# Performance work log

Hardware: AMD Instinct MI355X
Metric: run time of the kernel (lower is better)

## Reference

```python
import jax, jax.numpy as jnp
import numpy as np

N = 50000
E = 800000
F_IN = 128
HID = 16
HEADS = 8
C = 16
NEG_SLOPE = 0.2


def setup_inputs() -> dict:
    key = jax.random.key(0)
    ks = jax.random.split(key, 12)
    glorot = lambda k, shape: jax.random.normal(k, shape, jnp.float32) * jnp.sqrt(2.0 / (shape[0] + shape[-1]))
    return {
        "x": jax.random.normal(ks[0], (N, F_IN), jnp.float32),
        "edge_index": jax.random.randint(ks[1], (2, E), 0, N, jnp.int32),
        "x2": jax.random.normal(ks[2], (N, F_IN), jnp.float32),
        "edge_index2": jax.random.randint(ks[3], (2, E), 0, N, jnp.int32),
        # conv1: GATConv(F_IN -> HID, heads=HEADS, concat=True)
        "W1": glorot(ks[4], (F_IN, HEADS * HID)),
        "a1_src": glorot(ks[5], (HEADS, HID)),
        "a1_dst": glorot(ks[6], (HEADS, HID)),
        "b1": jnp.zeros((HEADS * HID,), jnp.float32),
        # conv2: GATConv(HEADS*HID -> C, heads=1, concat=False)
        "W2": glorot(ks[7], (HEADS * HID, 1 * C)),
        "a2_src": glorot(ks[8], (1, C)),
        "a2_dst": glorot(ks[9], (1, C)),
        "b2": jnp.zeros((C,), jnp.float32),
    }


def gat_conv(x, edge_index, W, a_src, a_dst, bias, concat):
    """PyG-style GATConv with self-loops, segment softmax over destinations."""
    n = x.shape[0]
    heads, out = a_src.shape
    h = (x @ W).reshape(n, heads, out)               # [N, H, O]
    loops = jnp.arange(n, dtype=edge_index.dtype)
    src = jnp.concatenate([edge_index[0], loops])     # messages flow src -> dst
    dst = jnp.concatenate([edge_index[1], loops])
    alpha_s = jnp.einsum('nho,ho->nh', h, a_src)
    alpha_d = jnp.einsum('nho,ho->nh', h, a_dst)
    e = jax.nn.leaky_relu(alpha_s[src] + alpha_d[dst], NEG_SLOPE)  # [E+N, H]
    m = jax.lax.stop_gradient(jax.ops.segment_max(e, dst, num_segments=n))
    w = jnp.exp(e - m[dst])
    denom = jax.ops.segment_sum(w, dst, num_segments=n)
    alpha = w / (denom[dst] + 1e-16)                  # segment softmax
    msg = h[src] * alpha[:, :, None]                  # [E+N, H, O]
    agg = jax.ops.segment_sum(msg, dst, num_segments=n)
    agg = agg.reshape(n, heads * out) if concat else agg.mean(axis=1)
    return agg + bias


def forward_once(x, edge_index, W1, a1_src, a1_dst, b1, W2, a2_src, a2_dst, b2):
    # dropout(p=0.6) is identity in eval mode
    h = jax.nn.elu(gat_conv(x, edge_index, W1, a1_src, a1_dst, b1, concat=True))
    return gat_conv(h, edge_index, W2, a2_src, a2_dst, b2, concat=False)


def reference(x, edge_index, x2, edge_index2, W1, a1_src, a1_dst, b1, W2, a2_src, a2_dst, b2):
    y = forward_once(x, edge_index, W1, a1_src, a1_dst, b1, W2, a2_src, a2_dst, b2)
    z = forward_once(x2, edge_index2, W1, a1_src, a1_dst, b1, W2, a2_src, a2_dst, b2)
    eps = 1e-8
    ny = jnp.maximum(jnp.linalg.norm(y, axis=1), eps)
    nz = jnp.maximum(jnp.linalg.norm(z, axis=1), eps)
    cos = jnp.sum(y * z, axis=1) / (ny * nz)
    ls_y = jax.nn.log_softmax(y, axis=1)
    ls_z = jax.nn.log_softmax(z, axis=1)
    return (ls_y, 1.0 - cos, ls_z, ls_y, ls_y)
```

## Files before the change

### kernel.cpp

```cpp
#include <hip/hip_runtime.h>
#include <hip/hip_bf16.h>

#define N_NODES 50000
#define N_EDGES 800000
#define F_INS   128
#define HIDDEN  16
#define HEADS   8
#define HO      128
#define C_OUT   16
#define NEG_SLOPE 0.2f
#define SLOT    64
#define NB_G1X  ((N_NODES + 31) / 32)
#define XSTR    132

#define NCLS     128
#define CLS_MUL  1342u
#define CLS_SH   19
#define CAP      8192
#define CHUNK    2048
#define NB_BKT   ((N_EDGES + CHUNK - 1) / CHUNK)

typedef unsigned short u16;
typedef unsigned int   u32;
typedef int v4i __attribute__((ext_vector_type(4)));

__device__ __forceinline__ float bf2f(u16 u) {
    union { u32 i; float f; } t; t.i = ((u32)u) << 16; return t.f;
}
__device__ __forceinline__ float bflo(u32 q) {
    union { u32 i; float f; } t; t.i = q << 16; return t.f;
}
__device__ __forceinline__ float bfhi(u32 q) {
    union { u32 i; float f; } t; t.i = q & 0xFFFF0000u; return t.f;
}
__device__ __forceinline__ u16 f2bf(float f) {
    union { float f; u32 i; } t; t.f = f;
    u32 x = t.i;
    u32 lsb = (x >> 16) & 1u;
    x += 0x7FFFu + lsb;
    return (u16)(x >> 16);
}
__device__ __forceinline__ int cls_of(int d) { return (int)(((u32)d * CLS_MUL) >> CLS_SH); }
__host__ __device__ __forceinline__ int cls_base(int c) { return (int)(((u32)c * 524288u + (CLS_MUL - 1)) / CLS_MUL); }

__launch_bounds__(256)
__global__ void k_bucket(const int* __restrict__ ei0, const int* __restrict__ ei1,
                         int* __restrict__ gcur, u32* __restrict__ bucket) {
    __shared__ int cnt[NCLS];
    __shared__ int base[NCLS];
    int t = threadIdx.x;
    int g = blockIdx.x & 1;
    int chunk = blockIdx.x >> 1;
    int e0 = chunk * CHUNK + t * 8;
    bool act = e0 < N_EDGES;

    if (t < NCLS) cnt[t] = 0;
    __syncthreads();

    const int* src = g ? ei1 : ei0;
    const int* dst = src + N_EDGES;
    int d8[8], s8[8], c8[8];
    if (act) {
        v4i da = *(const v4i*)(dst + e0), db = *(const v4i*)(dst + e0 + 4);
        v4i sa = *(const v4i*)(src + e0), sb = *(const v4i*)(src + e0 + 4);
        d8[0]=da[0]; d8[1]=da[1]; d8[2]=da[2]; d8[3]=da[3];
        d8[4]=db[0]; d8[5]=db[1]; d8[6]=db[2]; d8[7]=db[3];
        s8[0]=sa[0]; s8[1]=sa[1]; s8[2]=sa[2]; s8[3]=sa[3];
        s8[4]=sb[0]; s8[5]=sb[1]; s8[6]=sb[2]; s8[7]=sb[3];
        #pragma unroll
        for (int j = 0; j < 8; ++j) {
            c8[j] = cls_of(d8[j]);
            atomicAdd(&cnt[c8[j]], 1);
        }
    }
    __syncthreads();
    if (t < NCLS) {
        int n = cnt[t];
        base[t] = n ? atomicAdd(&gcur[g * NCLS + t], n) : 0;
        cnt[t] = 0;
    }
    __syncthreads();
    if (act) {
        #pragma unroll
        for (int j = 0; j < 8; ++j) {
            int c = c8[j];
            int p = atomicAdd(&cnt[c], 1);
            bucket[(size_t)(g * NCLS + c) * CAP + base[c] + p] =
                ((u32)d8[j] << 16) | (u32)s8[j];
        }
    }
}

__launch_bounds__(256)
__global__ void k_build(const int* __restrict__ gcur, const u32* __restrict__ bucket,
                        int* __restrict__ cursor, u16* __restrict__ col) {
    __shared__ int cnt[391];
    int t = threadIdx.x;
    int c = blockIdx.x & (NCLS - 1);
    int g = blockIdx.x >> 7;
    int d0 = cls_base(c);
    int d1 = (c == NCLS - 1) ? N_NODES : cls_base(c + 1);
    int nn = d1 - d0;
    for (int j = t; j < nn; j += 256) cnt[j] = 0;
    __syncthreads();

    int size = gcur[g * NCLS + c];
    const u32* bp = bucket + (size_t)(g * NCLS + c) * CAP;
    u16* cl = col + (size_t)g * N_NODES * SLOT;
    for (int i = t; i < size; i += 256) {
        u32 e = bp[i];
        int d = (int)(e >> 16);
        int s = (int)(e & 0xFFFFu);
        int p = atomicAdd(&cnt[d - d0], 1);
        if (p < SLOT) cl[(size_t)d * SLOT + p] = (u16)s;
    }
    __syncthreads();
    int* cur = cursor + g * N_NODES;
    for (int j = t; j < nn; j += 256) cur[d0 + j] = cnt[j];
}

__launch_bounds__(256)
__global__ void k_gemm1(const float* __restrict__ x, const float* __restrict__ W1,
                        const float* __restrict__ a1s, const float* __restrict__ a1d,
                        u32* __restrict__ h1b, float* __restrict__ as_,
                        float* __restrict__ ad_) {
    __shared__ float ws_[F_INS * 64];
    __shared__ float xs[32 * XSTR];
    int t = threadIdx.x;
    int half = blockIdx.y;

    const float4* w4 = (const float4*)W1;
    float4*       wl = (float4*)ws_;
    #pragma unroll
    for (int i = 0; i < 8; ++i) {
        int id2 = t + i * 256;
        int k = id2 >> 4;
        int c = id2 & 15;
        wl[id2] = w4[k * 32 + half * 16 + c];
    }

    int r0 = blockIdx.x * 32;
    const float4* x4 = (const float4*)x;
    #pragma unroll
    for (int i = 0; i < 4; ++i) {
        int id2 = t + i * 256;
        int r  = id2 >> 5;
        int c4 = id2 & 31;
        float4 q = make_float4(0.f, 0.f, 0.f, 0.f);
        if (r0 + r < N_NODES) q = x4[(size_t)(r0 + r) * 32 + c4];
        *(float4*)(xs + r * XSTR + c4 * 4) = q;
    }
    __syncthreads();

    int cg = t & 15;
    int rs = t >> 4;
    float acc[2][4];
    #pragma unroll
    for (int i = 0; i < 2; ++i)
        #pragma unroll
        for (int j = 0; j < 4; ++j) acc[i][j] = 0.f;

    #pragma unroll 8
    for (int k = 0; k < F_INS; ++k) {
        float4 wv = wl[k * 16 + cg];
        float xv0 = xs[rs * XSTR + k];
        float xv1 = xs[(rs + 16) * XSTR + k];
        acc[0][0] += xv0 * wv.x; acc[0][1] += xv0 * wv.y;
        acc[0][2] += xv0 * wv.z; acc[0][3] += xv0 * wv.w;
        acc[1][0] += xv1 * wv.x; acc[1][1] += xv1 * wv.y;
        acc[1][2] += xv1 * wv.z; acc[1][3] += xv1 * wv.w;
    }

    int gc = half * 64 + 4 * cg;
    int hglob = gc >> 4;
    float4 va = *(const float4*)(a1s + gc);
    float4 vd = *(const float4*)(a1d + gc);

    #pragma unroll
    for (int i = 0; i < 2; ++i) {
        int r = r0 + rs + 16 * i;
        float sa = acc[i][0]*va.x + acc[i][1]*va.y + acc[i][2]*va.z + acc[i][3]*va.w;
        float sd = acc[i][0]*vd.x + acc[i][1]*vd.y + acc[i][2]*vd.z + acc[i][3]*vd.w;
        sa += __shfl_xor(sa, 1); sa += __shfl_xor(sa, 2);
        sd += __shfl_xor(sd, 1); sd += __shfl_xor(sd, 2);
        if (r < N_NODES) {
            u32 p0 = ((u32)f2bf(acc[i][1]) << 16) | (u32)f2bf(acc[i][0]);
            u32 p1 = ((u32)f2bf(acc[i][3]) << 16) | (u32)f2bf(acc[i][2]);
            ((uint2*)h1b)[(size_t)r * 32 + half * 16 + cg] = make_uint2(p0, p1);
            if ((cg & 3) == 0) {
                as_[r * 8 + hglob] = sa;
                ad_[r * 8 + hglob] = sd;
            }
        }
    }
}

__launch_bounds__(256)
__global__ void k_gat1(const u32* __restrict__ h1b, const float* __restrict__ as_,
                       const float* __restrict__ ad_, const int* __restrict__ cursor,
                       const u16* __restrict__ col, const float* __restrict__ b1,
                       u32* __restrict__ hL1) {
    int lane = threadIdx.x & 63;
    int node = blockIdx.x * 4 + (threadIdx.x >> 6);
    if (node >= N_NODES) return;
    int h = lane >> 3;
    float ad = ad_[node * 8 + h];

    float as0 = as_[node * 8 + h];
    float tt = as0 + ad;
    tt = (tt > 0.f) ? tt : NEG_SLOPE * tt;
    float w = __expf(tt);
    float denom = w;
    u32 q = h1b[(size_t)node * 64 + lane];
    float ax = w * bflo(q), ay = w * bfhi(q);

    int deg = min(cursor[node], SLOT);
    const u16* cp = col + (size_t)node * SLOT;
    int e = 0;
    for (; e + 7 < deg; e += 8) {
        ushort4 sa4 = *(const ushort4*)(cp + e);
        ushort4 sb4 = *(const ushort4*)(cp + e + 4);
        int s0 = sa4.x, s1 = sa4.y, s2 = sa4.z, s3 = sa4.w;
        int s4 = sb4.x, s5 = sb4.y, s6 = sb4.z, s7 = sb4.w;
        float A0 = as_[s0 * 8 + h], A1 = as_[s1 * 8 + h];
        float A2 = as_[s2 * 8 + h], A3 = as_[s3 * 8 + h];
        float A4 = as_[s4 * 8 + h], A5 = as_[s5 * 8 + h];
        float A6 = as_[s6 * 8 + h], A7 = as_[s7 * 8 + h];
        u32 q0 = h1b[(size_t)s0 * 64 + lane], q1 = h1b[(size_t)s1 * 64 + lane];
        u32 q2 = h1b[(size_t)s2 * 64 + lane], q3 = h1b[(size_t)s3 * 64 + lane];
        u32 q4 = h1b[(size_t)s4 * 64 + lane], q5 = h1b[(size_t)s5 * 64 + lane];
        u32 q6 = h1b[(size_t)s6 * 64 + lane], q7 = h1b[(size_t)s7 * 64 + lane];
        float t0 = A0 + ad; t0 = (t0 > 0.f) ? t0 : NEG_SLOPE * t0;
        float t1 = A1 + ad; t1 = (t1 > 0.f) ? t1 : NEG_SLOPE * t1;
        float t2 = A2 + ad; t2 = (t2 > 0.f) ? t2 : NEG_SLOPE * t2;
        float t3 = A3 + ad; t3 = (t3 > 0.f) ? t3 : NEG_SLOPE * t3;
        float t4 = A4 + ad; t4 = (t4 > 0.f) ? t4 : NEG_SLOPE * t4;
        float t5 = A5 + ad; t5 = (t5 > 0.f) ? t5 : NEG_SLOPE * t5;
        float t6 = A6 + ad; t6 = (t6 > 0.f) ? t6 : NEG_SLOPE * t6;
        float t7 = A7 + ad; t7 = (t7 > 0.f) ? t7 : NEG_SLOPE * t7;
        float w0 = __expf(t0), w1 = __expf(t1), w2 = __expf(t2), w3 = __expf(t3);
        float w4 = __expf(t4), w5 = __expf(t5), w6 = __expf(t6), w7 = __expf(t7);
        denom += ((w0 + w1) + (w2 + w3)) + ((w4 + w5) + (w6 + w7));
        ax += w0 * bflo(q0) + w1 * bflo(q1) + w2 * bflo(q2) + w3 * bflo(q3)
            + w4 * bflo(q4) + w5 * bflo(q5) + w6 * bflo(q6) + w7 * bflo(q7);
        ay += w0 * bfhi(q0) + w1 * bfhi(q1) + w2 * bfhi(q2) + w3 * bfhi(q3)
            + w4 * bfhi(q4) + w5 * bfhi(q5) + w6 * bfhi(q6) + w7 * bfhi(q7);
    }
    for (; e + 3 < deg; e += 4) {
        ushort4 s4v = *(const ushort4*)(cp + e);
        int s0 = s4v.x, s1 = s4v.y, s2 = s4v.z, s3 = s4v.w;
        float A0 = as_[s0 * 8 + h], A1 = as_[s1 * 8 + h];
        float A2 = as_[s2 * 8 + h], A3 = as_[s3 * 8 + h];
        u32 q0 = h1b[(size_t)s0 * 64 + lane], q1 = h1b[(size_t)s1 * 64 + lane];
        u32 q2 = h1b[(size_t)s2 * 64 + lane], q3 = h1b[(size_t)s3 * 64 + lane];
        float t0 = A0 + ad; t0 = (t0 > 0.f) ? t0 : NEG_SLOPE * t0;
        float t1 = A1 + ad; t1 = (t1 > 0.f) ? t1 : NEG_SLOPE * t1;
        float t2 = A2 + ad; t2 = (t2 > 0.f) ? t2 : NEG_SLOPE * t2;
        float t3 = A3 + ad; t3 = (t3 > 0.f) ? t3 : NEG_SLOPE * t3;
        float w0 = __expf(t0), w1 = __expf(t1), w2 = __expf(t2), w3 = __expf(t3);
        denom += (w0 + w1) + (w2 + w3);
        ax += w0 * bflo(q0) + w1 * bflo(q1) + w2 * bflo(q2) + w3 * bflo(q3);
        ay += w0 * bfhi(q0) + w1 * bfhi(q1) + w2 * bfhi(q2) + w3 * bfhi(q3);
    }
    for (; e < deg; ++e) {
        int s = cp[e];
        float A = as_[s * 8 + h];
        u32 qq = h1b[(size_t)s * 64 + lane];
        float t0 = A + ad; t0 = (t0 > 0.f) ? t0 : NEG_SLOPE * t0;
        float w0 = __expf(t0);
        denom += w0;
        ax += w0 * bflo(qq);
        ay += w0 * bfhi(qq);
    }
    float inv = 1.f / (denom + 1e-16f);
    int c = lane * 2;
    float o0 = ax * inv + b1[c];
    float o1 = ay * inv + b1[c + 1];
    o0 = (o0 > 0.f) ? o0 : (__expf(o0) - 1.f);
    o1 = (o1 > 0.f) ? o1 : (__expf(o1) - 1.f);
    hL1[(size_t)node * 64 + lane] = ((u32)f2bf(o1) << 16) | (u32)f2bf(o0);
}

__launch_bounds__(256)
__global__ void k_gemm2(const u16* __restrict__ hL1, const float* __restrict__ W2,
                        const float* __restrict__ a2s, const float* __restrict__ a2d,
                        float* __restrict__ h2, float* __restrict__ as2,
                        float* __restrict__ ad2) {
    __shared__ float w2s[F_INS * C_OUT];
    __shared__ float hs[16 * 136];
    int t = threadIdx.x;

    const float4* w4 = (const float4*)W2;
    #pragma unroll
    for (int i = 0; i < 2; ++i) {
        int idx = t + i * 256;
        ((float4*)w2s)[idx] = w4[idx];
    }
    int r0 = blockIdx.x * 16;
    const ushort4* hg = (const ushort4*)hL1;
    #pragma unroll
    for (int i = 0; i < 2; ++i) {
        int idx = t + i * 256;
        int r  = idx >> 5;
        int c4 = idx & 31;
        ushort4 q = make_ushort4(0, 0, 0, 0);
        if (r0 + r < N_NODES) q = hg[(size_t)(r0 + r) * 32 + c4];
        float4 v; v.x = bf2f(q.x); v.y = bf2f(q.y); v.z = bf2f(q.z); v.w = bf2f(q.w);
        *(float4*)(hs + r * 136 + c4 * 4) = v;
    }
    __syncthreads();

    int c = t & 15, r = t >> 4;
    float acc = 0.f;
    #pragma unroll 8
    for (int k = 0; k < F_INS; ++k) acc += hs[r * 136 + k] * w2s[k * C_OUT + c];
    int n = r0 + r;
    if (n < N_NODES) h2[(size_t)n * C_OUT + c] = acc;

    float sa = acc * a2s[c];
    float sd = acc * a2d[c];
    #pragma unroll
    for (int m = 1; m < 16; m <<= 1) {
        sa += __shfl_xor(sa, m);
        sd += __shfl_xor(sd, m);
    }
    if (c == 0 && n < N_NODES) { as2[n] = sa; ad2[n] = sd; }
}

__device__ __forceinline__ void gat2_accum(const float* __restrict__ h2,
                                           const float* __restrict__ as2, float ad,
                                           const u16* __restrict__ cp, int deg, int c,
                                           float& denom, float& acc) {
    int e = 0;
    for (; e + 7 < deg; e += 8) {
        ushort4 sa4 = *(const ushort4*)(cp + e);
        ushort4 sb4 = *(const ushort4*)(cp + e + 4);
        int s0 = sa4.x, s1 = sa4.y, s2 = sa4.z, s3 = sa4.w;
        int s4 = sb4.x, s5 = sb4.y, s6 = sb4.z, s7 = sb4.w;
        float A0 = as2[s0], A1 = as2[s1], A2 = as2[s2], A3 = as2[s3];
        float A4 = as2[s4], A5 = as2[s5], A6 = as2[s6], A7 = as2[s7];
        float v0 = h2[(size_t)s0 * C_OUT + c], v1 = h2[(size_t)s1 * C_OUT + c];
        float v2 = h2[(size_t)s2 * C_OUT + c], v3 = h2[(size_t)s3 * C_OUT + c];
        float v4 = h2[(size_t)s4 * C_OUT + c], v5 = h2[(size_t)s5 * C_OUT + c];
        float v6 = h2[(size_t)s6 * C_OUT + c], v7 = h2[(size_t)s7 * C_OUT + c];
        float t0 = A0 + ad; t0 = (t0 > 0.f) ? t0 : NEG_SLOPE * t0;
        float t1 = A1 + ad; t1 = (t1 > 0.f) ? t1 : NEG_SLOPE * t1;
        float t2 = A2 + ad; t2 = (t2 > 0.f) ? t2 : NEG_SLOPE * t2;
        float t3 = A3 + ad; t3 = (t3 > 0.f) ? t3 : NEG_SLOPE * t3;
        float t4 = A4 + ad; t4 = (t4 > 0.f) ? t4 : NEG_SLOPE * t4;
        float t5 = A5 + ad; t5 = (t5 > 0.f) ? t5 : NEG_SLOPE * t5;
        float t6 = A6 + ad; t6 = (t6 > 0.f) ? t6 : NEG_SLOPE * t6;
        float t7 = A7 + ad; t7 = (t7 > 0.f) ? t7 : NEG_SLOPE * t7;
        float w0 = __expf(t0), w1 = __expf(t1), w2 = __expf(t2), w3 = __expf(t3);
        float w4 = __expf(t4), w5 = __expf(t5), w6 = __expf(t6), w7 = __expf(t7);
        denom += ((w0 + w1) + (w2 + w3)) + ((w4 + w5) + (w6 + w7));
        acc += (w0 * v0 + w1 * v1 + w2 * v2 + w3 * v3)
             + (w4 * v4 + w5 * v5 + w6 * v6 + w7 * v7);
    }
    for (; e + 3 < deg; e += 4) {
        ushort4 s4v = *(const ushort4*)(cp + e);
        int s0 = s4v.x, s1 = s4v.y, s2 = s4v.z, s3 = s4v.w;
        float A0 = as2[s0], A1 = as2[s1], A2 = as2[s2], A3 = as2[s3];
        float v0 = h2[(size_t)s0 * C_OUT + c], v1 = h2[(size_t)s1 * C_OUT + c];
        float v2 = h2[(size_t)s2 * C_OUT + c], v3 = h2[(size_t)s3 * C_OUT + c];
        float t0 = A0 + ad; t0 = (t0 > 0.f) ? t0 : NEG_SLOPE * t0;
        float t1 = A1 + ad; t1 = (t1 > 0.f) ? t1 : NEG_SLOPE * t1;
        float t2 = A2 + ad; t2 = (t2 > 0.f) ? t2 : NEG_SLOPE * t2;
        float t3 = A3 + ad; t3 = (t3 > 0.f) ? t3 : NEG_SLOPE * t3;
        float w0 = __expf(t0), w1 = __expf(t1), w2 = __expf(t2), w3 = __expf(t3);
        denom += (w0 + w1) + (w2 + w3);
        acc += w0 * v0 + w1 * v1 + w2 * v2 + w3 * v3;
    }
    for (; e < deg; ++e) {
        int s = cp[e];
        float t0 = as2[s] + ad; t0 = (t0 > 0.f) ? t0 : NEG_SLOPE * t0;
        float w0 = __expf(t0);
        denom += w0;
        acc += w0 * h2[(size_t)s * C_OUT + c];
    }
}

__launch_bounds__(256)
__global__ void k_gat2(const float* __restrict__ h2, const float* __restrict__ as2,
                       const float* __restrict__ ad2, const int* __restrict__ cursor,
                       const u16* __restrict__ col, const float* __restrict__ b2,
                       float* __restrict__ yout) {
    int t = threadIdx.x;
    int node = blockIdx.x * 16 + (t >> 4);
    int c = t & 15;
    if (node >= N_NODES) return;
    float ad = ad2[node];

    float tt = as2[node] + ad;
    tt = (tt > 0.f) ? tt : NEG_SLOPE * tt;
    float w = __expf(tt);
    float denom = w;
    float acc = w * h2[(size_t)node * C_OUT + c];

    int deg = min(cursor[node], SLOT);
    gat2_accum(h2, as2, ad, col + (size_t)node * SLOT, deg, c, denom, acc);
    yout[(size_t)node * C_OUT + c] = acc / (denom + 1e-16f) + b2[c];
}

__launch_bounds__(256)
__global__ void k_gat2f(const float* __restrict__ h2, const float* __restrict__ as2,
                        const float* __restrict__ ad2, const int* __restrict__ cursor,
                        const u16* __restrict__ col, const float* __restrict__ b2,
                        const float* __restrict__ yb, float* __restrict__ out) {
    int t = threadIdx.x;
    int node = blockIdx.x * 16 + (t >> 4);
    int c = t & 15;
    if (node >= N_NODES) return;
    float ad = ad2[node];

    float tt = as2[node] + ad;
    tt = (tt > 0.f) ? tt : NEG_SLOPE * tt;
    float w = __expf(tt);
    float denom = w;
    float acc = w * h2[(size_t)node * C_OUT + c];

    int deg = min(cursor[node], SLOT);
    gat2_accum(h2, as2, ad, col + (size_t)node * SLOT, deg, c, denom, acc);
    float zv = acc / (denom + 1e-16f) + b2[c];
    float yv = yb[(size_t)node * C_OUT + c];

    float my = yv, mz = zv;
    #pragma unroll
    for (int m = 1; m < 16; m <<= 1) {
        my = fmaxf(my, __shfl_xor(my, m));
        mz = fmaxf(mz, __shfl_xor(mz, m));
    }
    float sy = __expf(yv - my), sz = __expf(zv - mz);
    float dot = yv * zv, ny = yv * yv, nz = zv * zv;
    #pragma unroll
    for (int m = 1; m < 16; m <<= 1) {
        sy  += __shfl_xor(sy, m);
        sz  += __shfl_xor(sz, m);
        dot += __shfl_xor(dot, m);
        ny  += __shfl_xor(ny, m);
        nz  += __shfl_xor(nz, m);
    }
    float lsey = my + __logf(sy);
    float lsez = mz + __logf(sz);
    float omc = 1.f - dot / (fmaxf(sqrtf(ny), 1e-8f) * fmaxf(sqrtf(nz), 1e-8f));

    const int O1 = N_NODES * C_OUT;
    const int O2 = O1 + N_NODES;
    const int O3 = O2 + N_NODES * C_OUT;
    const int O4 = O3 + N_NODES * C_OUT;
    float ly = yv - lsey;
    float lz = zv - lsez;
    int base = node * 16 + c;
    out[base]      = ly;
    out[O2 + base] = lz;
    out[O3 + base] = ly;
    out[O4 + base] = ly;
    if (c == 0) out[O1 + node] = omc;
}

extern "C" void kernel_launch(void* const* d_in, const int* in_sizes, int n_in,
                              void* d_out, int out_size, void* d_ws, size_t ws_size,
                              hipStream_t stream) {
    (void)in_sizes; (void)n_in; (void)out_size; (void)ws_size;
    const float* x1  = (const float*)d_in[0];
    const int*   ei1 = (const int*)d_in[1];
    const float* x2  = (const float*)d_in[2];
    const int*   ei2 = (const int*)d_in[3];
    const float* W1  = (const float*)d_in[4];
    const float* a1s = (const float*)d_in[5];
    const float* a1d = (const float*)d_in[6];
    const float* b1  = (const float*)d_in[7];
    const float* W2  = (const float*)d_in[8];
    const float* a2s = (const float*)d_in[9];
    const float* a2d = (const float*)d_in[10];
    const float* b2  = (const float*)d_in[11];
    float* out = (float*)d_out;

    char* p = (char*)d_ws;
    int* gcur      = (int*)p; p += (size_t)2 * NCLS * 4;
    int* cursor    = (int*)p; p += (size_t)2 * N_NODES * 4;
    u16* col       = (u16*)p; p += (size_t)2 * N_NODES * SLOT * 2;
    float* as1  = (float*)p; p += (size_t)N_NODES * HEADS * 4;
    float* ad1  = (float*)p; p += (size_t)N_NODES * HEADS * 4;
    float* h2   = (float*)p; p += (size_t)N_NODES * C_OUT * 4;
    float* as2  = (float*)p; p += (size_t)N_NODES * 4;
    float* ad2  = (float*)p; p += (size_t)N_NODES * 4;
    float* yb   = (float*)p; p += (size_t)N_NODES * C_OUT * 4;
    u32* hL1    = (u32*)p;   p += (size_t)N_NODES * HO * 2;
    u32* h1b    = (u32*)p;   p += (size_t)N_NODES * HO * 2;
    u32* bucket = h1b;

    hipMemsetAsync(gcur, 0, (size_t)2 * NCLS * 4, stream);
    k_bucket<<<2 * NB_BKT, 256, 0, stream>>>(ei1, ei2, gcur, bucket);
    k_build <<<2 * NCLS, 256, 0, stream>>>(gcur, bucket, cursor, col);

    for (int g = 0; g < 2; ++g) {
        const float* x = g ? x2 : x1;
        int* cur_g = cursor + g * N_NODES;
        u16* col_g = col + (size_t)g * N_NODES * SLOT;
        dim3 g1(NB_G1X, 2);
        k_gemm1<<<g1, 256, 0, stream>>>(x, W1, a1s, a1d, h1b, as1, ad1);
        k_gat1 <<<(N_NODES + 3) / 4, 256, 0, stream>>>(h1b, as1, ad1, cur_g, col_g, b1, hL1);
        k_gemm2<<<(N_NODES + 15) / 16, 256, 0, stream>>>((const u16*)hL1, W2, a2s, a2d, h2, as2, ad2);
        if (g == 0) {
            k_gat2 <<<(N_NODES + 15) / 16, 256, 0, stream>>>(h2, as2, ad2, cur_g, col_g, b2, yb);
        } else {
            k_gat2f<<<(N_NODES + 15) / 16, 256, 0, stream>>>(h2, as2, ad2, cur_g, col_g, b2, yb, out);
        }
    }
}
```

Baseline: 342.9 us.

## Compute first-layer GEMM with bf16 MFMA and fold attention vectors into weights

Replaces the fp32 SIMT GEMM for layer 1 with a bf16 MFMA 16x16x32 kernel. A small prep kernel transposes and packs W1 to bf16 and precomputes W1·a_src and W1·a_dst as an extra 16-column tile, so the attention logits come straight out of the same MFMA pass. Each block now handles 64 rows across all 128 columns, so x is read once instead of twice. In exchange, x and the attention projections are rounded to bf16, which lowers accuracy of the attention scores.

```diff
diff --git a/kernel.cpp b/kernel.cpp
--- a/kernel.cpp
+++ b/kernel.cpp
@@ -10,8 +10,7 @@
 #define C_OUT   16
 #define NEG_SLOPE 0.2f
 #define SLOT    64
-#define NB_G1X  ((N_NODES + 31) / 32)
-#define XSTR    132
+#define NB_G1   ((N_NODES + 63) / 64)
 
 #define NCLS     128
 #define CLS_MUL  1342u
@@ -23,6 +22,8 @@
 typedef unsigned short u16;
 typedef unsigned int   u32;
 typedef int v4i __attribute__((ext_vector_type(4)));
+typedef short bf16x8 __attribute__((ext_vector_type(8)));
+typedef float f32x4 __attribute__((ext_vector_type(4)));
 
 __device__ __forceinline__ float bf2f(u16 u) {
     union { u32 i; float f; } t; t.i = ((u32)u) << 16; return t.f;
@@ -33,15 +34,43 @@
 __device__ __forceinline__ float bfhi(u32 q) {
     union { u32 i; float f; } t; t.i = q & 0xFFFF0000u; return t.f;
 }
-__device__ __forceinline__ u16 f2bf(float f) {
+__device__ __forceinline__ u32 f2bf(float f) {
     union { float f; u32 i; } t; t.f = f;
     u32 x = t.i;
     u32 lsb = (x >> 16) & 1u;
     x += 0x7FFFu + lsb;
-    return (u16)(x >> 16);
+    return x >> 16;
 }
 __device__ __forceinline__ int cls_of(int d) { return (int)(((u32)d * CLS_MUL) >> CLS_SH); }
 __host__ __device__ __forceinline__ int cls_base(int c) { return (int)(((u32)c * 524288u + (CLS_MUL - 1)) / CLS_MUL); }
+
+__global__ void k_wt(const float* __restrict__ W1, const float* __restrict__ a1s,
+                     const float* __restrict__ a1d, u32* __restrict__ w1t,
+                     u32* __restrict__ a1t) {
+    int t = threadIdx.x;
+    if (blockIdx.x < 32) {
+        int e = blockIdx.x * 256 + t;
+        int c = e >> 6, kp = e & 63;
+        float lo = W1[(2 * kp) * 128 + c];
+        float hi = W1[(2 * kp + 1) * 128 + c];
+        w1t[e] = (f2bf(hi) << 16) | f2bf(lo);
+    } else {
+        #pragma unroll
+        for (int i = 0; i < 4; ++i) {
+            int wi = t + i * 256;
+            int n = wi >> 6, kp = wi & 63;
+            int h = n >> 1;
+            const float* av = ((n & 1) ? a1d : a1s) + h * 16;
+            float s0 = 0.f, s1 = 0.f;
+            #pragma unroll
+            for (int c = 0; c < 16; ++c) {
+                s0 += W1[(2 * kp) * 128 + h * 16 + c] * av[c];
+                s1 += W1[(2 * kp + 1) * 128 + h * 16 + c] * av[c];
+            }
+            a1t[wi] = (f2bf(s1) << 16) | f2bf(s0);
+        }
+    }
+}
 
 __launch_bounds__(256)
 __global__ void k_bucket(const int* __restrict__ ei0, const int* __restrict__ ei1,
@@ -120,77 +149,67 @@
 }
 
 __launch_bounds__(256)
-__global__ void k_gemm1(const float* __restrict__ x, const float* __restrict__ W1,
-                        const float* __restrict__ a1s, const float* __restrict__ a1d,
-                        u32* __restrict__ h1b, float* __restrict__ as_,
-                        float* __restrict__ ad_) {
-    __shared__ float ws_[F_INS * 64];
-    __shared__ float xs[32 * XSTR];
-    int t = threadIdx.x;
-    int half = blockIdx.y;
-
-    const float4* w4 = (const float4*)W1;
-    float4*       wl = (float4*)ws_;
-    #pragma unroll
-    for (int i = 0; i < 8; ++i) {
-        int id2 = t + i * 256;
-        int k = id2 >> 4;
-        int c = id2 & 15;
-        wl[id2] = w4[k * 32 + half * 16 + c];
-    }
-
-    int r0 = blockIdx.x * 32;
-    const float4* x4 = (const float4*)x;
-    #pragma unroll
-    for (int i = 0; i < 4; ++i) {
-        int id2 = t + i * 256;
-        int r  = id2 >> 5;
-        int c4 = id2 & 31;
-        float4 q = make_float4(0.f, 0.f, 0.f, 0.f);
-        if (r0 + r < N_NODES) q = x4[(size_t)(r0 + r) * 32 + c4];
-        *(float4*)(xs + r * XSTR + c4 * 4) = q;
-    }
-    __syncthreads();
-
-    int cg = t & 15;
-    int rs = t >> 4;
-    float acc[2][4];
-    #pragma unroll
-    for (int i = 0; i < 2; ++i)
+__global__ void k_gemm1(const float* __restrict__ x, const u32* __restrict__ w1t,
+                        const u32* __restrict__ a1t, u32* __restrict__ h1b,
+                        float* __restrict__ as_, float* __restrict__ ad_) {
+    __shared__ u32 xls[4096];
+    int t = threadIdx.x;
+    int r0 = blockIdx.x * 64;
+
+    const float2* x2p = (const float2*)x;
+    #pragma unroll
+    for (int i = 0; i < 16; ++i) {
+        int A = t + i * 256;
+        int wi = A >> 10, kt = (A >> 8) & 3, L = (A >> 2) & 63, jj = A & 3;
+        int m = L & 15, qd = L >> 4;
+        int r = r0 + wi * 16 + m;
+        int pp = kt * 16 + qd * 4 + jj;
+        float2 v = make_float2(0.f, 0.f);
+        if (r < N_NODES) v = x2p[(size_t)r * 64 + pp];
+        xls[A] = (f2bf(v.y) << 16) | f2bf(v.x);
+    }
+    __syncthreads();
+
+    int lane = t & 63;
+    int wid = t >> 6;
+    int n = lane & 15, quad = lane >> 4;
+
+    f32x4 acc[8], acca;
+    #pragma unroll
+    for (int ct = 0; ct < 8; ++ct) acc[ct] = (f32x4){0.f, 0.f, 0.f, 0.f};
+    acca = (f32x4){0.f, 0.f, 0.f, 0.f};
+
+    #pragma unroll
+    for (int kt = 0; kt < 4; ++kt) {
+        union { uint4 u; bf16x8 v; } af;
+        af.u = *(const uint4*)(xls + wid * 1024 + kt * 256 + lane * 4);
         #pragma unroll
-        for (int j = 0; j < 4; ++j) acc[i][j] = 0.f;
-
-    #pragma unroll 8
-    for (int k = 0; k < F_INS; ++k) {
-        float4 wv = wl[k * 16 + cg];
-        float xv0 = xs[rs * XSTR + k];
-        float xv1 = xs[(rs + 16) * XSTR + k];
-        acc[0][0] += xv0 * wv.x; acc[0][1] += xv0 * wv.y;
-        acc[0][2] += xv0 * wv.z; acc[0][3] += xv0 * wv.w;
-        acc[1][0] += xv1 * wv.x; acc[1][1] += xv1 * wv.y;
-        acc[1][2] += xv1 * wv.z; acc[1][3] += xv1 * wv.w;
-    }
-
-    int gc = half * 64 + 4 * cg;
-    int hglob = gc >> 4;
-    float4 va = *(const float4*)(a1s + gc);
-    float4 vd = *(const float4*)(a1d + gc);
-
-    #pragma unroll
-    for (int i = 0; i < 2; ++i) {
-        int r = r0 + rs + 16 * i;
-        float sa = acc[i][0]*va.x + acc[i][1]*va.y + acc[i][2]*va.z + acc[i][3]*va.w;
-        float sd = acc[i][0]*vd.x + acc[i][1]*vd.y + acc[i][2]*vd.z + acc[i][3]*vd.w;
-        sa += __shfl_xor(sa, 1); sa += __shfl_xor(sa, 2);
-        sd += __shfl_xor(sd, 1); sd += __shfl_xor(sd, 2);
-        if (r < N_NODES) {
-            u32 p0 = ((u32)f2bf(acc[i][1]) << 16) | (u32)f2bf(acc[i][0]);
-            u32 p1 = ((u32)f2bf(acc[i][3]) << 16) | (u32)f2bf(acc[i][2]);
-            ((uint2*)h1b)[(size_t)r * 32 + half * 16 + cg] = make_uint2(p0, p1);
-            if ((cg & 3) == 0) {
-                as_[r * 8 + hglob] = sa;
-                ad_[r * 8 + hglob] = sd;
-            }
+        for (int ct = 0; ct < 8; ++ct) {
+            union { uint4 u; bf16x8 v; } bf_;
+            bf_.u = *(const uint4*)(w1t + (ct * 16 + n) * 64 + kt * 16 + quad * 4);
+            acc[ct] = __builtin_amdgcn_mfma_f32_16x16x32_bf16(af.v, bf_.v, acc[ct], 0, 0, 0);
+        }
+        union { uint4 u; bf16x8 v; } ba;
+        ba.u = *(const uint4*)(a1t + n * 64 + kt * 16 + quad * 4);
+        acca = __builtin_amdgcn_mfma_f32_16x16x32_bf16(af.v, ba.v, acca, 0, 0, 0);
+    }
+
+    int h = n >> 1;
+    #pragma unroll
+    for (int reg = 0; reg < 4; ++reg) {
+        int gr = r0 + wid * 16 + quad * 4 + reg;
+        bool ok = gr < N_NODES;
+        float av = acca[reg];
+        if (ok) {
+            if (n & 1) ad_[gr * 8 + h] = av;
+            else       as_[gr * 8 + h] = av;
+        }
+        #pragma unroll
+        for (int ct = 0; ct < 8; ++ct) {
+            u32 my = f2bf(acc[ct][reg]);
+            u32 ot = (u32)__shfl_xor((int)my, 1);
+            if (!(n & 1) && ok)
+                h1b[(size_t)gr * 64 + ct * 8 + (n >> 1)] = (ot << 16) | my;
         }
     }
 }
@@ -278,7 +297,7 @@
     float o1 = ay * inv + b1[c + 1];
     o0 = (o0 > 0.f) ? o0 : (__expf(o0) - 1.f);
     o1 = (o1 > 0.f) ? o1 : (__expf(o1) - 1.f);
-    hL1[(size_t)node * 64 + lane] = ((u32)f2bf(o1) << 16) | (u32)f2bf(o0);
+    hL1[(size_t)node * 64 + lane] = (f2bf(o1) << 16) | f2bf(o0);
 }
 
 __launch_bounds__(256)
@@ -478,6 +497,8 @@
 
     char* p = (char*)d_ws;
     int* gcur      = (int*)p; p += (size_t)2 * NCLS * 4;
+    u32* w1t       = (u32*)p; p += (size_t)128 * 64 * 4;
+    u32* a1t       = (u32*)p; p += (size_t)16 * 64 * 4;
     int* cursor    = (int*)p; p += (size_t)2 * N_NODES * 4;
     u16* col       = (u16*)p; p += (size_t)2 * N_NODES * SLOT * 2;
     float* as1  = (float*)p; p += (size_t)N_NODES * HEADS * 4;
@@ -491,6 +512,7 @@
     u32* bucket = h1b;
 
     hipMemsetAsync(gcur, 0, (size_t)2 * NCLS * 4, stream);
+    k_wt    <<<33, 256, 0, stream>>>(W1, a1s, a1d, w1t, a1t);
     k_bucket<<<2 * NB_BKT, 256, 0, stream>>>(ei1, ei2, gcur, bucket);
     k_build <<<2 * NCLS, 256, 0, stream>>>(gcur, bucket, cursor, col);
 
@@ -498,8 +520,7 @@
         const float* x = g ? x2 : x1;
         int* cur_g = cursor + g * N_NODES;
         u16* col_g = col + (size_t)g * N_NODES * SLOT;
-        dim3 g1(NB_G1X, 2);
-        k_gemm1<<<g1, 256, 0, stream>>>(x, W1, a1s, a1d, h1b, as1, ad1);
+        k_gemm1<<<NB_G1, 256, 0, stream>>>(x, w1t, a1t, h1b, as1, ad1);
         k_gat1 <<<(N_NODES + 3) / 4, 256, 0, stream>>>(h1b, as1, ad1, cur_g, col_g, b1, hL1);
         k_gemm2<<<(N_NODES + 15) / 16, 256, 0, stream>>>((const u16*)hL1, W2, a2s, a2d, h2, as2, ad2);
         if (g == 0) {
```

After: 341.9 us. About the same (-0.3%).
